# Kernel tuning notes

Measured on AMD Instinct MI355X. Metric: run time of the kernel, lower is better.

Reference implementation:

```python
import jax, jax.numpy as jnp
import numpy as np

B, L, DM, H, DK, DV = 8, 1024, 512, 8, 64, 64
LN_EPS = 1e-5

def setup_inputs() -> dict:
    key = jax.random.key(0)
    ks = jax.random.split(key, 8)
    s_in = 1.0 / np.sqrt(DM)
    return {
        "q": jax.random.normal(ks[0], (B, L, DM), jnp.float32),
        "k": jax.random.normal(ks[1], (B, L, DM), jnp.float32),
        "v": jax.random.normal(ks[2], (B, L, DM), jnp.float32),
        "Wq": jax.random.normal(ks[3], (DM, H * DK), jnp.float32) * s_in,
        "bq": jnp.zeros((H * DK,), jnp.float32),
        "Wk": jax.random.normal(ks[4], (DM, H * DK), jnp.float32) * s_in,
        "bk": jnp.zeros((H * DK,), jnp.float32),
        "Wv": jax.random.normal(ks[5], (DM, H * DV), jnp.float32) * s_in,
        "bv": jnp.zeros((H * DV,), jnp.float32),
        "Wmap": jax.random.normal(ks[6], (2 * DK, 1), jnp.float32) * (1.0 / np.sqrt(2 * DK)),
        "bmap": jnp.zeros((1,), jnp.float32),
        "Wfc": jax.random.normal(ks[7], (H * DV, DM), jnp.float32) * (1.0 / np.sqrt(H * DV)),
        "bfc": jnp.zeros((DM,), jnp.float32),
        "ln_scale": jnp.ones((DM,), jnp.float32),
        "ln_bias": jnp.zeros((DM,), jnp.float32),
    }

def reference(q, k, v, Wq, bq, Wk, bk, Wv, bv, Wmap, bmap, Wfc, bfc, ln_scale, ln_bias):
    sz_b, len_q, _ = q.shape
    len_k = k.shape[1]
    residual = q
    # projections -> (H, B, L, d)
    qh = (q @ Wq + bq).reshape(sz_b, len_q, H, DK).transpose(2, 0, 1, 3)
    kh = (k @ Wk + bk).reshape(sz_b, len_k, H, DK).transpose(2, 0, 1, 3)
    vh = (v @ Wv + bv).reshape(sz_b, len_k, H, DV).transpose(2, 0, 1, 3)
    # additive score: Linear(concat(q,k)) == q@Wmap[:DK] + k@Wmap[DK:] + b
    # (avoids materializing the (H*B, Lq, Lk, 2*DK) concat; same math)
    sq = qh @ Wmap[:DK, 0]   # (H, B, Lq)
    sk = kh @ Wmap[DK:, 0]   # (H, B, Lk)
    scores = sq[..., :, None] + sk[..., None, :] + bmap[0]  # (H, B, Lq, Lk)
    attn = jax.nn.softmax(scores, axis=-1)
    out = jnp.einsum('hbqk,hbkd->hbqd', attn, vh)            # (H, B, Lq, DV)
    out = out.transpose(1, 2, 0, 3).reshape(sz_b, len_q, H * DV)
    out = out @ Wfc + bfc + residual
    mu = out.mean(-1, keepdims=True)
    var = out.var(-1, keepdims=True)
    out = (out - mu) / jnp.sqrt(var + LN_EPS) * ln_scale + ln_bias
    return out, attn.reshape(H * sz_b, len_q, len_k)
```

## Files before the change

kernel.cpp:

```cpp
#include <hip/hip_runtime.h>
#include <cstdint>
#include <cstddef>

#define B 8
#define L 1024
#define DM 512
#define H 8
#define LN_EPS 1e-5f

#define U_OFF    0
#define SK_OFF   8192
#define PART_OFF 81920
#define CTX_OFF  344064
#define OBP_OFF  348160

#define OUT_ELEMS ((size_t)B * L * DM)

typedef float f4 __attribute__((ext_vector_type(4)));

__device__ __forceinline__ float wave_sum(float s) {
#pragma unroll
    for (int off = 32; off > 0; off >>= 1) s += __shfl_xor(s, off, 64);
    return s;
}

__global__ __launch_bounds__(64) void k_prep(const float* __restrict__ Wk,
                                             const float* __restrict__ Wmap,
                                             float* __restrict__ ws) {
    __shared__ float wm[64];
    int t = threadIdx.x;
    wm[t] = Wmap[64 + t];
    __syncthreads();
    int h = t >> 3, part = t & 7;
#pragma unroll
    for (int i = 0; i < 8; ++i) {
        int dm = blockIdx.x * 8 + i;
        const float* row = Wk + (size_t)dm * (H * 64) + h * 64 + part * 8;
        float s = 0.f;
#pragma unroll
        for (int d = 0; d < 8; ++d) s += row[d] * wm[part * 8 + d];
        s += __shfl_xor(s, 1, 64);
        s += __shfl_xor(s, 2, 64);
        s += __shfl_xor(s, 4, 64);
        if (part == 0) ws[U_OFF + dm * H + h] = s;
    }
}

__global__ __launch_bounds__(256) void k_sk(const float* __restrict__ k,
                                            float* __restrict__ ws) {
    int wave = threadIdx.x >> 6, lane = threadIdx.x & 63;
    int row = blockIdx.x * 4 + wave;
    int b = row >> 10, l = row & 1023;
    const float* krow = k + (size_t)row * DM;
    const float* u = ws + U_OFF;
    float acc[8] = {0, 0, 0, 0, 0, 0, 0, 0};
#pragma unroll
    for (int s8 = 0; s8 < 8; ++s8) {
        int dm = s8 * 64 + lane;
        float kv = krow[dm];
        const float4 ua = *(const float4*)(u + dm * 8);
        const float4 ub = *(const float4*)(u + dm * 8 + 4);
        acc[0] += kv * ua.x; acc[1] += kv * ua.y;
        acc[2] += kv * ua.z; acc[3] += kv * ua.w;
        acc[4] += kv * ub.x; acc[5] += kv * ub.y;
        acc[6] += kv * ub.z; acc[7] += kv * ub.w;
    }
#pragma unroll
    for (int off = 32; off > 0; off >>= 1) {
#pragma unroll
        for (int h = 0; h < 8; ++h) acc[h] += __shfl_xor(acc[h], off, 64);
    }
    float vout = 0.f;
#pragma unroll
    for (int h = 0; h < 8; ++h) if (lane == h) vout = acc[h];
    if (lane < 8)
        ws[SK_OFF + ((size_t)(lane * B + b)) * L + l] = vout;
}

__global__ __launch_bounds__(256) void k_vbar(const float* __restrict__ v,
                                              float* __restrict__ ws) {
    __shared__ float ps[H][128];
    int blk = blockIdx.x;
    int chunk = blk & 7, b = (blk >> 3) & 7, js = blk >> 6;
    int w = threadIdx.x >> 6, lane = threadIdx.x & 63;
#pragma unroll
    for (int rep = 0; rep < 2; ++rep) {
        int h = w * 2 + rep;
        const float* rowp = ws + SK_OFF + ((size_t)(h * B + b)) * L;
        float e[16];
        const f4* r4 = (const f4*)(rowp + lane * 16);
        float part = 0.f;
#pragma unroll
        for (int i = 0; i < 4; ++i) {
            f4 x = r4[i];
            e[i * 4 + 0] = __expf(x.x); e[i * 4 + 1] = __expf(x.y);
            e[i * 4 + 2] = __expf(x.z); e[i * 4 + 3] = __expf(x.w);
            part += e[i * 4 + 0] + e[i * 4 + 1] + e[i * 4 + 2] + e[i * 4 + 3];
        }
        float s = wave_sum(part);
        float inv = 1.f / s;
        float2 seg = *(const float2*)(rowp + js * 128 + lane * 2);
        ps[h][lane * 2 + 0] = __expf(seg.x) * inv;
        ps[h][lane * 2 + 1] = __expf(seg.y) * inv;
    }
    __syncthreads();
    int dm = chunk * 64 + lane;
    const float* vb0 = v + ((size_t)b * L + js * 128) * DM + dm;
    int h0 = w * 2;
    float a0 = 0.f, a1 = 0.f;
#pragma unroll 4
    for (int jj = 0; jj < 128; ++jj) {
        float vv = vb0[(size_t)jj * DM];
        a0 += ps[h0][jj] * vv;
        a1 += ps[h0 + 1][jj] * vv;
    }
    ws[PART_OFF + ((size_t)((js * H + h0) * B + b)) * DM + dm] = a0;
    ws[PART_OFF + ((size_t)((js * H + h0 + 1) * B + b)) * DM + dm] = a1;
}

__global__ __launch_bounds__(256) void k_ctx(const float* __restrict__ Wv,
                                             const float* __restrict__ bv,
                                             float* __restrict__ ws) {
    __shared__ float vb[DM];
    __shared__ float red[4][64];
    int hb = blockIdx.x;
    int h = hb >> 3, b = hb & 7;
#pragma unroll
    for (int it = 0; it < 2; ++it) {
        int dm = threadIdx.x + it * 256;
        float s = 0.f;
#pragma unroll
        for (int js = 0; js < 8; ++js)
            s += ws[PART_OFF + ((size_t)((js * H + h) * B + b)) * DM + dm];
        vb[dm] = s;
    }
    __syncthreads();
    int w = threadIdx.x >> 6, d = threadIdx.x & 63;
    float acc = 0.f;
#pragma unroll 4
    for (int i = 0; i < 128; ++i) {
        int dm = w * 128 + i;
        acc += vb[dm] * Wv[(size_t)dm * DM + h * 64 + d];
    }
    red[w][d] = acc;
    __syncthreads();
    if (w == 0) {
        float r = red[0][d] + red[1][d] + red[2][d] + red[3][d] + bv[h * 64 + d];
        ws[CTX_OFF + (size_t)b * DM + h * 64 + d] = r;
    }
}

__global__ __launch_bounds__(512) void k_obase(const float* __restrict__ Wfc,
                                               float* __restrict__ ws) {
    __shared__ float cxs[64];
    int b = blockIdx.x & 7, ms = blockIdx.x >> 3;
    if (threadIdx.x < 64)
        cxs[threadIdx.x] = ws[CTX_OFF + (size_t)b * DM + ms * 64 + threadIdx.x];
    __syncthreads();
    int n = threadIdx.x;
    float acc = 0.f;
#pragma unroll 4
    for (int m = 0; m < 64; ++m)
        acc += cxs[m] * Wfc[(size_t)(ms * 64 + m) * DM + n];
    ws[OBP_OFF + (size_t)(ms * B + b) * DM + n] = acc;
}

__global__ __launch_bounds__(256) void k_out(const float* __restrict__ q,
                                             const float* __restrict__ bfc,
                                             const float* __restrict__ lns,
                                             const float* __restrict__ lnb,
                                             const float* __restrict__ ws,
                                             float* __restrict__ out) {
    __shared__ float obf[DM];
    int b = blockIdx.x >> 8;
    for (int i = threadIdx.x; i < DM; i += 256) {
        float s = bfc[i];
#pragma unroll
        for (int ms = 0; ms < 8; ++ms)
            s += ws[OBP_OFF + (size_t)(ms * B + b) * DM + i];
        obf[i] = s;
    }
    __syncthreads();
    int wave = threadIdx.x >> 6, lane = threadIdx.x & 63;
    int row = blockIdx.x * 4 + wave;
    const float* qr = q + (size_t)row * DM;
    int d0 = lane * 8;
    float4 a = *(const float4*)(qr + d0);
    float4 c = *(const float4*)(qr + d0 + 4);
    float x[8] = {a.x + obf[d0],     a.y + obf[d0 + 1],
                  a.z + obf[d0 + 2], a.w + obf[d0 + 3],
                  c.x + obf[d0 + 4], c.y + obf[d0 + 5],
                  c.z + obf[d0 + 6], c.w + obf[d0 + 7]};
    float sum = 0.f, sq = 0.f;
#pragma unroll
    for (int i = 0; i < 8; ++i) { sum += x[i]; sq += x[i] * x[i]; }
#pragma unroll
    for (int off = 32; off > 0; off >>= 1) {
        sum += __shfl_xor(sum, off, 64);
        sq  += __shfl_xor(sq,  off, 64);
    }
    float mu = sum * (1.f / DM);
    float var = sq * (1.f / DM) - mu * mu;
    float inv = rsqrtf(var + LN_EPS);
    float4 sa = *(const float4*)(lns + d0);
    float4 sc = *(const float4*)(lns + d0 + 4);
    float4 ba = *(const float4*)(lnb + d0);
    float4 bb = *(const float4*)(lnb + d0 + 4);
    float sarr[8] = {sa.x, sa.y, sa.z, sa.w, sc.x, sc.y, sc.z, sc.w};
    float barr[8] = {ba.x, ba.y, ba.z, ba.w, bb.x, bb.y, bb.z, bb.w};
    float y[8];
#pragma unroll
    for (int i = 0; i < 8; ++i) y[i] = (x[i] - mu) * inv * sarr[i] + barr[i];
    float4 o0 = {y[0], y[1], y[2], y[3]};
    float4 o1 = {y[4], y[5], y[6], y[7]};
    *(float4*)(out + (size_t)row * DM + d0) = o0;
    *(float4*)(out + (size_t)row * DM + d0 + 4) = o1;
}

__global__ __launch_bounds__(256) void k_attn(const float* __restrict__ ws,
                                              float* __restrict__ out) {
    __shared__ float red[4];
    int hb = blockIdx.x >> 6;
    int ic = blockIdx.x & 63;
    int t = threadIdx.x, wave = t >> 6, lane = t & 63;
    float4 s4 = *(const float4*)&ws[SK_OFF + (size_t)hb * L + t * 4];
    float e0 = __expf(s4.x), e1 = __expf(s4.y), e2 = __expf(s4.z), e3 = __expf(s4.w);
    float s = wave_sum(e0 + e1 + e2 + e3);
    if (lane == 0) red[wave] = s;
    __syncthreads();
    float inv = 1.f / (red[0] + red[1] + red[2] + red[3]);
    f4 p4 = {e0 * inv, e1 * inv, e2 * inv, e3 * inv};
    float* base = out + OUT_ELEMS + ((size_t)hb * L + (size_t)ic * 16) * L + t * 4;
#pragma unroll
    for (int r = 0; r < 16; ++r)
        __builtin_nontemporal_store(p4, (f4*)(base + (size_t)r * L));
}

extern "C" void kernel_launch(void* const* d_in, const int* in_sizes, int n_in,
                              void* d_out, int out_size, void* d_ws, size_t ws_size,
                              hipStream_t stream) {
    const float* q    = (const float*)d_in[0];
    const float* k    = (const float*)d_in[1];
    const float* v    = (const float*)d_in[2];
    const float* Wk   = (const float*)d_in[5];
    const float* Wv   = (const float*)d_in[7];
    const float* bv   = (const float*)d_in[8];
    const float* Wmap = (const float*)d_in[9];
    const float* Wfc  = (const float*)d_in[11];
    const float* bfc  = (const float*)d_in[12];
    const float* lns  = (const float*)d_in[13];
    const float* lnb  = (const float*)d_in[14];
    float* out = (float*)d_out;
    float* ws  = (float*)d_ws;

    hipLaunchKernelGGL(k_prep,  dim3(64),   dim3(64),  0, stream, Wk, Wmap, ws);
    hipLaunchKernelGGL(k_sk,    dim3(2048), dim3(256), 0, stream, k, ws);
    hipLaunchKernelGGL(k_vbar,  dim3(512),  dim3(256), 0, stream, v, ws);
    hipLaunchKernelGGL(k_ctx,   dim3(64),   dim3(256), 0, stream, Wv, bv, ws);
    hipLaunchKernelGGL(k_obase, dim3(64),   dim3(512), 0, stream, Wfc, ws);
    hipLaunchKernelGGL(k_out,   dim3(2048), dim3(256), 0, stream, q, bfc, lns, lnb, ws, out);
    hipLaunchKernelGGL(k_attn,  dim3(4096), dim3(256), 0, stream, ws, out);
}
```

Before: 110.6 us.

## Fuse vbar, ctx, obase, out and attn into one persistent kernel with atomic counters

Merges five dependent kernels into a single launch. Block ranges run different stages, and dependent stages spin on global atomic counters set by earlier block groups. The streaming attention-matrix write blocks sit between the producer and the final LayerNorm blocks, so their memory traffic can overlap the small serial GEMV chain. This removes launch gaps. In exchange it relies on blocks being dispatched in index order to avoid deadlock, and it adds spin-wait latency. The LayerNorm blocks now handle 16 rows each instead of 4.

```diff
diff --git a/kernel.cpp b/kernel.cpp
--- a/kernel.cpp
+++ b/kernel.cpp
@@ -9,6 +9,7 @@
 #define LN_EPS 1e-5f
 
 #define U_OFF    0
+#define CNT_OFF  4096
 #define SK_OFF   8192
 #define PART_OFF 81920
 #define CTX_OFF  344064
@@ -22,6 +23,20 @@
 #pragma unroll
     for (int off = 32; off > 0; off >>= 1) s += __shfl_xor(s, off, 64);
     return s;
+}
+
+__device__ __forceinline__ void wait_cnt(int* cnt, int target) {
+    if (threadIdx.x == 0) {
+        while (__hip_atomic_load(cnt, __ATOMIC_RELAXED, __HIP_MEMORY_SCOPE_AGENT) < target)
+            __builtin_amdgcn_s_sleep(8);
+    }
+    __syncthreads();
+    __builtin_amdgcn_fence(__ATOMIC_ACQUIRE, "agent");
+}
+__device__ __forceinline__ void signal_cnt(int* cnt) {
+    __syncthreads();
+    if (threadIdx.x == 0)
+        __hip_atomic_fetch_add(cnt, 1, __ATOMIC_RELEASE, __HIP_MEMORY_SCOPE_AGENT);
 }
 
 __global__ __launch_bounds__(64) void k_prep(const float* __restrict__ Wk,
@@ -29,6 +44,7 @@
                                              float* __restrict__ ws) {
     __shared__ float wm[64];
     int t = threadIdx.x;
+    if (blockIdx.x == 0 && t < 3) ((int*)(ws + CNT_OFF))[t] = 0;
     wm[t] = Wmap[64 + t];
     __syncthreads();
     int h = t >> 3, part = t & 7;
@@ -77,163 +93,158 @@
         ws[SK_OFF + ((size_t)(lane * B + b)) * L + l] = vout;
 }
 
-__global__ __launch_bounds__(256) void k_vbar(const float* __restrict__ v,
-                                              float* __restrict__ ws) {
-    __shared__ float ps[H][128];
+__global__ __launch_bounds__(256) void k_mega(
+    const float* __restrict__ q, const float* __restrict__ v,
+    const float* __restrict__ Wv, const float* __restrict__ bv,
+    const float* __restrict__ Wfc, const float* __restrict__ bfc,
+    const float* __restrict__ lns, const float* __restrict__ lnb,
+    float* __restrict__ ws, float* __restrict__ out)
+{
+    __shared__ float smem[1032];
+    int* cnt = (int*)(ws + CNT_OFF);
     int blk = blockIdx.x;
-    int chunk = blk & 7, b = (blk >> 3) & 7, js = blk >> 6;
-    int w = threadIdx.x >> 6, lane = threadIdx.x & 63;
-#pragma unroll
-    for (int rep = 0; rep < 2; ++rep) {
-        int h = w * 2 + rep;
-        const float* rowp = ws + SK_OFF + ((size_t)(h * B + b)) * L;
-        float e[16];
-        const f4* r4 = (const f4*)(rowp + lane * 16);
-        float part = 0.f;
-#pragma unroll
-        for (int i = 0; i < 4; ++i) {
-            f4 x = r4[i];
-            e[i * 4 + 0] = __expf(x.x); e[i * 4 + 1] = __expf(x.y);
-            e[i * 4 + 2] = __expf(x.z); e[i * 4 + 3] = __expf(x.w);
-            part += e[i * 4 + 0] + e[i * 4 + 1] + e[i * 4 + 2] + e[i * 4 + 3];
-        }
-        float s = wave_sum(part);
-        float inv = 1.f / s;
-        float2 seg = *(const float2*)(rowp + js * 128 + lane * 2);
-        ps[h][lane * 2 + 0] = __expf(seg.x) * inv;
-        ps[h][lane * 2 + 1] = __expf(seg.y) * inv;
-    }
-    __syncthreads();
-    int dm = chunk * 64 + lane;
-    const float* vb0 = v + ((size_t)b * L + js * 128) * DM + dm;
-    int h0 = w * 2;
-    float a0 = 0.f, a1 = 0.f;
+    int t = threadIdx.x, wave = t >> 6, lane = t & 63;
+
+    if (blk < 512) {
+        int chunk = blk & 7, b = (blk >> 3) & 7, js = blk >> 6;
+#pragma unroll
+        for (int rep = 0; rep < 2; ++rep) {
+            int h = wave * 2 + rep;
+            const float* rowp = ws + SK_OFF + ((size_t)(h * B + b)) * L;
+            const f4* r4 = (const f4*)(rowp + lane * 16);
+            float part = 0.f;
+#pragma unroll
+            for (int i = 0; i < 4; ++i) {
+                f4 x = r4[i];
+                part += __expf(x.x) + __expf(x.y) + __expf(x.z) + __expf(x.w);
+            }
+            float s = wave_sum(part);
+            float inv = 1.f / s;
+            float2 seg = *(const float2*)(rowp + js * 128 + lane * 2);
+            smem[h * 128 + lane * 2 + 0] = __expf(seg.x) * inv;
+            smem[h * 128 + lane * 2 + 1] = __expf(seg.y) * inv;
+        }
+        __syncthreads();
+        int dm = chunk * 64 + lane;
+        const float* vb0 = v + ((size_t)b * L + js * 128) * DM + dm;
+        int h0 = wave * 2;
+        float a0 = 0.f, a1 = 0.f;
 #pragma unroll 4
-    for (int jj = 0; jj < 128; ++jj) {
-        float vv = vb0[(size_t)jj * DM];
-        a0 += ps[h0][jj] * vv;
-        a1 += ps[h0 + 1][jj] * vv;
-    }
-    ws[PART_OFF + ((size_t)((js * H + h0) * B + b)) * DM + dm] = a0;
-    ws[PART_OFF + ((size_t)((js * H + h0 + 1) * B + b)) * DM + dm] = a1;
-}
-
-__global__ __launch_bounds__(256) void k_ctx(const float* __restrict__ Wv,
-                                             const float* __restrict__ bv,
-                                             float* __restrict__ ws) {
-    __shared__ float vb[DM];
-    __shared__ float red[4][64];
-    int hb = blockIdx.x;
-    int h = hb >> 3, b = hb & 7;
-#pragma unroll
-    for (int it = 0; it < 2; ++it) {
-        int dm = threadIdx.x + it * 256;
-        float s = 0.f;
-#pragma unroll
-        for (int js = 0; js < 8; ++js)
-            s += ws[PART_OFF + ((size_t)((js * H + h) * B + b)) * DM + dm];
-        vb[dm] = s;
-    }
-    __syncthreads();
-    int w = threadIdx.x >> 6, d = threadIdx.x & 63;
-    float acc = 0.f;
+        for (int jj = 0; jj < 128; ++jj) {
+            float vv = vb0[(size_t)jj * DM];
+            a0 += smem[h0 * 128 + jj] * vv;
+            a1 += smem[(h0 + 1) * 128 + jj] * vv;
+        }
+        ws[PART_OFF + ((size_t)((js * H + h0) * B + b)) * DM + dm] = a0;
+        ws[PART_OFF + ((size_t)((js * H + h0 + 1) * B + b)) * DM + dm] = a1;
+        signal_cnt(cnt + 0);
+    } else if (blk < 576) {
+        wait_cnt(cnt + 0, 512);
+        int hb = blk - 512;
+        int h = hb >> 3, b = hb & 7;
+#pragma unroll
+        for (int it = 0; it < 2; ++it) {
+            int dm = t + it * 256;
+            float s = 0.f;
+#pragma unroll
+            for (int js = 0; js < 8; ++js)
+                s += ws[PART_OFF + ((size_t)((js * H + h) * B + b)) * DM + dm];
+            smem[dm] = s;
+        }
+        __syncthreads();
+        float acc = 0.f;
 #pragma unroll 4
-    for (int i = 0; i < 128; ++i) {
-        int dm = w * 128 + i;
-        acc += vb[dm] * Wv[(size_t)dm * DM + h * 64 + d];
-    }
-    red[w][d] = acc;
-    __syncthreads();
-    if (w == 0) {
-        float r = red[0][d] + red[1][d] + red[2][d] + red[3][d] + bv[h * 64 + d];
-        ws[CTX_OFF + (size_t)b * DM + h * 64 + d] = r;
-    }
-}
-
-__global__ __launch_bounds__(512) void k_obase(const float* __restrict__ Wfc,
-                                               float* __restrict__ ws) {
-    __shared__ float cxs[64];
-    int b = blockIdx.x & 7, ms = blockIdx.x >> 3;
-    if (threadIdx.x < 64)
-        cxs[threadIdx.x] = ws[CTX_OFF + (size_t)b * DM + ms * 64 + threadIdx.x];
-    __syncthreads();
-    int n = threadIdx.x;
-    float acc = 0.f;
+        for (int i = 0; i < 128; ++i) {
+            int dm = wave * 128 + i;
+            acc += smem[dm] * Wv[(size_t)dm * DM + h * 64 + lane];
+        }
+        smem[512 + wave * 64 + lane] = acc;
+        __syncthreads();
+        if (wave == 0) {
+            float r = smem[512 + lane] + smem[576 + lane] + smem[640 + lane]
+                    + smem[704 + lane] + bv[h * 64 + lane];
+            ws[CTX_OFF + (size_t)b * DM + h * 64 + lane] = r;
+        }
+        signal_cnt(cnt + 1);
+    } else if (blk < 640) {
+        wait_cnt(cnt + 1, 64);
+        int idx = blk - 576;
+        int b = idx & 7, ms = idx >> 3;
+        if (t < 64) smem[t] = ws[CTX_OFF + (size_t)b * DM + ms * 64 + t];
+        __syncthreads();
+#pragma unroll
+        for (int it = 0; it < 2; ++it) {
+            int n = t + it * 256;
+            float acc = 0.f;
 #pragma unroll 4
-    for (int m = 0; m < 64; ++m)
-        acc += cxs[m] * Wfc[(size_t)(ms * 64 + m) * DM + n];
-    ws[OBP_OFF + (size_t)(ms * B + b) * DM + n] = acc;
-}
-
-__global__ __launch_bounds__(256) void k_out(const float* __restrict__ q,
-                                             const float* __restrict__ bfc,
-                                             const float* __restrict__ lns,
-                                             const float* __restrict__ lnb,
-                                             const float* __restrict__ ws,
-                                             float* __restrict__ out) {
-    __shared__ float obf[DM];
-    int b = blockIdx.x >> 8;
-    for (int i = threadIdx.x; i < DM; i += 256) {
-        float s = bfc[i];
-#pragma unroll
-        for (int ms = 0; ms < 8; ++ms)
-            s += ws[OBP_OFF + (size_t)(ms * B + b) * DM + i];
-        obf[i] = s;
-    }
-    __syncthreads();
-    int wave = threadIdx.x >> 6, lane = threadIdx.x & 63;
-    int row = blockIdx.x * 4 + wave;
-    const float* qr = q + (size_t)row * DM;
-    int d0 = lane * 8;
-    float4 a = *(const float4*)(qr + d0);
-    float4 c = *(const float4*)(qr + d0 + 4);
-    float x[8] = {a.x + obf[d0],     a.y + obf[d0 + 1],
-                  a.z + obf[d0 + 2], a.w + obf[d0 + 3],
-                  c.x + obf[d0 + 4], c.y + obf[d0 + 5],
-                  c.z + obf[d0 + 6], c.w + obf[d0 + 7]};
-    float sum = 0.f, sq = 0.f;
-#pragma unroll
-    for (int i = 0; i < 8; ++i) { sum += x[i]; sq += x[i] * x[i]; }
-#pragma unroll
-    for (int off = 32; off > 0; off >>= 1) {
-        sum += __shfl_xor(sum, off, 64);
-        sq  += __shfl_xor(sq,  off, 64);
-    }
-    float mu = sum * (1.f / DM);
-    float var = sq * (1.f / DM) - mu * mu;
-    float inv = rsqrtf(var + LN_EPS);
-    float4 sa = *(const float4*)(lns + d0);
-    float4 sc = *(const float4*)(lns + d0 + 4);
-    float4 ba = *(const float4*)(lnb + d0);
-    float4 bb = *(const float4*)(lnb + d0 + 4);
-    float sarr[8] = {sa.x, sa.y, sa.z, sa.w, sc.x, sc.y, sc.z, sc.w};
-    float barr[8] = {ba.x, ba.y, ba.z, ba.w, bb.x, bb.y, bb.z, bb.w};
-    float y[8];
-#pragma unroll
-    for (int i = 0; i < 8; ++i) y[i] = (x[i] - mu) * inv * sarr[i] + barr[i];
-    float4 o0 = {y[0], y[1], y[2], y[3]};
-    float4 o1 = {y[4], y[5], y[6], y[7]};
-    *(float4*)(out + (size_t)row * DM + d0) = o0;
-    *(float4*)(out + (size_t)row * DM + d0 + 4) = o1;
-}
-
-__global__ __launch_bounds__(256) void k_attn(const float* __restrict__ ws,
-                                              float* __restrict__ out) {
-    __shared__ float red[4];
-    int hb = blockIdx.x >> 6;
-    int ic = blockIdx.x & 63;
-    int t = threadIdx.x, wave = t >> 6, lane = t & 63;
-    float4 s4 = *(const float4*)&ws[SK_OFF + (size_t)hb * L + t * 4];
-    float e0 = __expf(s4.x), e1 = __expf(s4.y), e2 = __expf(s4.z), e3 = __expf(s4.w);
-    float s = wave_sum(e0 + e1 + e2 + e3);
-    if (lane == 0) red[wave] = s;
-    __syncthreads();
-    float inv = 1.f / (red[0] + red[1] + red[2] + red[3]);
-    f4 p4 = {e0 * inv, e1 * inv, e2 * inv, e3 * inv};
-    float* base = out + OUT_ELEMS + ((size_t)hb * L + (size_t)ic * 16) * L + t * 4;
-#pragma unroll
-    for (int r = 0; r < 16; ++r)
-        __builtin_nontemporal_store(p4, (f4*)(base + (size_t)r * L));
+            for (int m = 0; m < 64; ++m)
+                acc += smem[m] * Wfc[(size_t)(ms * 64 + m) * DM + n];
+            ws[OBP_OFF + (size_t)(ms * B + b) * DM + n] = acc;
+        }
+        signal_cnt(cnt + 2);
+    } else if (blk < 4736) {
+        int task = blk - 640;
+        int hb = task >> 6, ic = task & 63;
+        float4 s4 = *(const float4*)&ws[SK_OFF + (size_t)hb * L + t * 4];
+        float e0 = __expf(s4.x), e1 = __expf(s4.y), e2 = __expf(s4.z), e3 = __expf(s4.w);
+        float s = wave_sum(e0 + e1 + e2 + e3);
+        if (lane == 0) smem[1024 + wave] = s;
+        __syncthreads();
+        float inv = 1.f / (smem[1024] + smem[1025] + smem[1026] + smem[1027]);
+        f4 p4 = {e0 * inv, e1 * inv, e2 * inv, e3 * inv};
+        float* base = out + OUT_ELEMS + ((size_t)hb * L + (size_t)ic * 16) * L + t * 4;
+#pragma unroll
+        for (int r = 0; r < 16; ++r)
+            __builtin_nontemporal_store(p4, (f4*)(base + (size_t)r * L));
+    } else {
+        wait_cnt(cnt + 2, 64);
+        int rblk = blk - 4736;
+        int b = rblk >> 6;
+        for (int i = t; i < DM; i += 256) {
+            float s = bfc[i];
+#pragma unroll
+            for (int ms = 0; ms < 8; ++ms)
+                s += ws[OBP_OFF + (size_t)(ms * B + b) * DM + i];
+            smem[i] = s;
+        }
+        __syncthreads();
+#pragma unroll
+        for (int rep = 0; rep < 4; ++rep) {
+            int row = rblk * 16 + rep * 4 + wave;
+            const float* qr = q + (size_t)row * DM;
+            int d0 = lane * 8;
+            float4 a = *(const float4*)(qr + d0);
+            float4 c = *(const float4*)(qr + d0 + 4);
+            float x[8] = {a.x + smem[d0],     a.y + smem[d0 + 1],
+                          a.z + smem[d0 + 2], a.w + smem[d0 + 3],
+                          c.x + smem[d0 + 4], c.y + smem[d0 + 5],
+                          c.z + smem[d0 + 6], c.w + smem[d0 + 7]};
+            float sum = 0.f, sq = 0.f;
+#pragma unroll
+            for (int i = 0; i < 8; ++i) { sum += x[i]; sq += x[i] * x[i]; }
+#pragma unroll
+            for (int off = 32; off > 0; off >>= 1) {
+                sum += __shfl_xor(sum, off, 64);
+                sq  += __shfl_xor(sq,  off, 64);
+            }
+            float mu = sum * (1.f / DM);
+            float var = sq * (1.f / DM) - mu * mu;
+            float invs = rsqrtf(var + LN_EPS);
+            float4 sa = *(const float4*)(lns + d0);
+            float4 sc = *(const float4*)(lns + d0 + 4);
+            float4 ba = *(const float4*)(lnb + d0);
+            float4 bb = *(const float4*)(lnb + d0 + 4);
+            float sarr[8] = {sa.x, sa.y, sa.z, sa.w, sc.x, sc.y, sc.z, sc.w};
+            float barr[8] = {ba.x, ba.y, ba.z, ba.w, bb.x, bb.y, bb.z, bb.w};
+            float y[8];
+#pragma unroll
+            for (int i = 0; i < 8; ++i) y[i] = (x[i] - mu) * invs * sarr[i] + barr[i];
+            float4 o0 = {y[0], y[1], y[2], y[3]};
+            float4 o1 = {y[4], y[5], y[6], y[7]};
+            *(float4*)(out + (size_t)row * DM + d0) = o0;
+            *(float4*)(out + (size_t)row * DM + d0 + 4) = o1;
+        }
+    }
 }
 
 extern "C" void kernel_launch(void* const* d_in, const int* in_sizes, int n_in,
@@ -253,11 +264,8 @@
     float* out = (float*)d_out;
     float* ws  = (float*)d_ws;
 
-    hipLaunchKernelGGL(k_prep,  dim3(64),   dim3(64),  0, stream, Wk, Wmap, ws);
-    hipLaunchKernelGGL(k_sk,    dim3(2048), dim3(256), 0, stream, k, ws);
-    hipLaunchKernelGGL(k_vbar,  dim3(512),  dim3(256), 0, stream, v, ws);
-    hipLaunchKernelGGL(k_ctx,   dim3(64),   dim3(256), 0, stream, Wv, bv, ws);
-    hipLaunchKernelGGL(k_obase, dim3(64),   dim3(512), 0, stream, Wfc, ws);
-    hipLaunchKernelGGL(k_out,   dim3(2048), dim3(256), 0, stream, q, bfc, lns, lnb, ws, out);
-    hipLaunchKernelGGL(k_attn,  dim3(4096), dim3(256), 0, stream, ws, out);
-}
+    hipLaunchKernelGGL(k_prep, dim3(64),   dim3(64),  0, stream, Wk, Wmap, ws);
+    hipLaunchKernelGGL(k_sk,   dim3(2048), dim3(256), 0, stream, k, ws);
+    hipLaunchKernelGGL(k_mega, dim3(5248), dim3(256), 0, stream,
+                       q, v, Wv, bv, Wfc, bfc, lns, lnb, ws, out);
+}
```

Measured after the change: 168.2 us. 1.52x slower.

## Merge attention-map writes into dependent stages and fuse ctx/obase kernels

Applied to the files above, without the earlier changes.

The standalone attention-probability store kernel is split into chunks of tasks appended to the vbar, ctx/fc and layernorm kernels as extra blocks. The small, low-occupancy stages then run alongside the bandwidth-bound attention writes instead of serializing. The ctx and obase kernels are fused into one kernel, with each block redundantly computing the full context vector for its batch. The layernorm kernel now processes 16 rows per block. Seven launches drop to five. The risk is the redundant Wv GEMV work in each of the 64 blocks and load imbalance between the two block types in each kernel.

```diff
diff --git a/kernel.cpp b/kernel.cpp
--- a/kernel.cpp
+++ b/kernel.cpp
@@ -11,8 +11,7 @@
 #define U_OFF    0
 #define SK_OFF   8192
 #define PART_OFF 81920
-#define CTX_OFF  344064
-#define OBP_OFF  348160
+#define OB_OFF   344064
 
 #define OUT_ELEMS ((size_t)B * L * DM)
 
@@ -22,6 +21,23 @@
 #pragma unroll
     for (int off = 32; off > 0; off >>= 1) s += __shfl_xor(s, off, 64);
     return s;
+}
+
+__device__ __forceinline__ void attn_task(int task, const float* __restrict__ ws,
+                                          float* __restrict__ out, float* red) {
+    int hb = task >> 6, ic = task & 63;
+    int t = threadIdx.x, wave = t >> 6, lane = t & 63;
+    float4 s4 = *(const float4*)&ws[SK_OFF + (size_t)hb * L + t * 4];
+    float e0 = __expf(s4.x), e1 = __expf(s4.y), e2 = __expf(s4.z), e3 = __expf(s4.w);
+    float s = wave_sum(e0 + e1 + e2 + e3);
+    if (lane == 0) red[wave] = s;
+    __syncthreads();
+    float inv = 1.f / (red[0] + red[1] + red[2] + red[3]);
+    f4 p4 = {e0 * inv, e1 * inv, e2 * inv, e3 * inv};
+    float* base = out + OUT_ELEMS + ((size_t)hb * L + (size_t)ic * 16) * L + t * 4;
+#pragma unroll
+    for (int r = 0; r < 16; ++r)
+        __builtin_nontemporal_store(p4, (f4*)(base + (size_t)r * L));
 }
 
 __global__ __launch_bounds__(64) void k_prep(const float* __restrict__ Wk,
@@ -77,163 +93,153 @@
         ws[SK_OFF + ((size_t)(lane * B + b)) * L + l] = vout;
 }
 
-__global__ __launch_bounds__(256) void k_vbar(const float* __restrict__ v,
-                                              float* __restrict__ ws) {
-    __shared__ float ps[H][128];
+__global__ __launch_bounds__(256) void k_l3(const float* __restrict__ v,
+                                            float* __restrict__ ws,
+                                            float* __restrict__ out) {
+    __shared__ float smem[1028];
     int blk = blockIdx.x;
-    int chunk = blk & 7, b = (blk >> 3) & 7, js = blk >> 6;
-    int w = threadIdx.x >> 6, lane = threadIdx.x & 63;
-#pragma unroll
-    for (int rep = 0; rep < 2; ++rep) {
-        int h = w * 2 + rep;
-        const float* rowp = ws + SK_OFF + ((size_t)(h * B + b)) * L;
-        float e[16];
-        const f4* r4 = (const f4*)(rowp + lane * 16);
-        float part = 0.f;
-#pragma unroll
-        for (int i = 0; i < 4; ++i) {
-            f4 x = r4[i];
-            e[i * 4 + 0] = __expf(x.x); e[i * 4 + 1] = __expf(x.y);
-            e[i * 4 + 2] = __expf(x.z); e[i * 4 + 3] = __expf(x.w);
-            part += e[i * 4 + 0] + e[i * 4 + 1] + e[i * 4 + 2] + e[i * 4 + 3];
-        }
-        float s = wave_sum(part);
-        float inv = 1.f / s;
-        float2 seg = *(const float2*)(rowp + js * 128 + lane * 2);
-        ps[h][lane * 2 + 0] = __expf(seg.x) * inv;
-        ps[h][lane * 2 + 1] = __expf(seg.y) * inv;
-    }
-    __syncthreads();
-    int dm = chunk * 64 + lane;
-    const float* vb0 = v + ((size_t)b * L + js * 128) * DM + dm;
-    int h0 = w * 2;
-    float a0 = 0.f, a1 = 0.f;
+    int t = threadIdx.x, wave = t >> 6, lane = t & 63;
+    if (blk < 512) {
+        int chunk = blk & 7, b = (blk >> 3) & 7, js = blk >> 6;
+#pragma unroll
+        for (int rep = 0; rep < 2; ++rep) {
+            int h = wave * 2 + rep;
+            const float* rowp = ws + SK_OFF + ((size_t)(h * B + b)) * L;
+            const f4* r4 = (const f4*)(rowp + lane * 16);
+            float part = 0.f;
+#pragma unroll
+            for (int i = 0; i < 4; ++i) {
+                f4 x = r4[i];
+                part += __expf(x.x) + __expf(x.y) + __expf(x.z) + __expf(x.w);
+            }
+            float s = wave_sum(part);
+            float inv = 1.f / s;
+            float2 seg = *(const float2*)(rowp + js * 128 + lane * 2);
+            smem[h * 128 + lane * 2 + 0] = __expf(seg.x) * inv;
+            smem[h * 128 + lane * 2 + 1] = __expf(seg.y) * inv;
+        }
+        __syncthreads();
+        int dm = chunk * 64 + lane;
+        const float* vb0 = v + ((size_t)b * L + js * 128) * DM + dm;
+        int h0 = wave * 2;
+        float a0 = 0.f, a1 = 0.f;
 #pragma unroll 4
-    for (int jj = 0; jj < 128; ++jj) {
-        float vv = vb0[(size_t)jj * DM];
-        a0 += ps[h0][jj] * vv;
-        a1 += ps[h0 + 1][jj] * vv;
-    }
-    ws[PART_OFF + ((size_t)((js * H + h0) * B + b)) * DM + dm] = a0;
-    ws[PART_OFF + ((size_t)((js * H + h0 + 1) * B + b)) * DM + dm] = a1;
-}
-
-__global__ __launch_bounds__(256) void k_ctx(const float* __restrict__ Wv,
-                                             const float* __restrict__ bv,
-                                             float* __restrict__ ws) {
-    __shared__ float vb[DM];
+        for (int jj = 0; jj < 128; ++jj) {
+            float vv = vb0[(size_t)jj * DM];
+            a0 += smem[h0 * 128 + jj] * vv;
+            a1 += smem[(h0 + 1) * 128 + jj] * vv;
+        }
+        ws[PART_OFF + ((size_t)((js * H + h0) * B + b)) * DM + dm] = a0;
+        ws[PART_OFF + ((size_t)((js * H + h0 + 1) * B + b)) * DM + dm] = a1;
+    } else {
+        attn_task(blk - 512, ws, out, smem + 1024);
+    }
+}
+
+__global__ __launch_bounds__(256) void k_l4(const float* __restrict__ Wv,
+                                            const float* __restrict__ bv,
+                                            const float* __restrict__ Wfc,
+                                            const float* __restrict__ bfc,
+                                            float* __restrict__ ws,
+                                            float* __restrict__ out) {
+    __shared__ float vbs[4096];
+    __shared__ float ctxs[512];
     __shared__ float red[4][64];
-    int hb = blockIdx.x;
-    int h = hb >> 3, b = hb & 7;
-#pragma unroll
-    for (int it = 0; it < 2; ++it) {
-        int dm = threadIdx.x + it * 256;
-        float s = 0.f;
-#pragma unroll
-        for (int js = 0; js < 8; ++js)
-            s += ws[PART_OFF + ((size_t)((js * H + h) * B + b)) * DM + dm];
-        vb[dm] = s;
-    }
-    __syncthreads();
-    int w = threadIdx.x >> 6, d = threadIdx.x & 63;
-    float acc = 0.f;
+    int blk = blockIdx.x;
+    int t = threadIdx.x;
+    if (blk < 64) {
+        int b = blk >> 3, ns = blk & 7;
+        for (int i = t; i < 4096; i += 256) {
+            int h = i >> 9, dm = i & 511;
+            float s = 0.f;
+#pragma unroll
+            for (int js = 0; js < 8; ++js)
+                s += ws[PART_OFF + ((size_t)((js * H + h) * B + b)) * DM + dm];
+            vbs[i] = s;
+        }
+        __syncthreads();
+#pragma unroll
+        for (int mo = 0; mo < 2; ++mo) {
+            int m = t + mo * 256;
+            const float* vh = &vbs[(m >> 6) << 9];
+            float acc = bv[m];
 #pragma unroll 4
-    for (int i = 0; i < 128; ++i) {
-        int dm = w * 128 + i;
-        acc += vb[dm] * Wv[(size_t)dm * DM + h * 64 + d];
-    }
-    red[w][d] = acc;
-    __syncthreads();
-    if (w == 0) {
-        float r = red[0][d] + red[1][d] + red[2][d] + red[3][d] + bv[h * 64 + d];
-        ws[CTX_OFF + (size_t)b * DM + h * 64 + d] = r;
-    }
-}
-
-__global__ __launch_bounds__(512) void k_obase(const float* __restrict__ Wfc,
-                                               float* __restrict__ ws) {
-    __shared__ float cxs[64];
-    int b = blockIdx.x & 7, ms = blockIdx.x >> 3;
-    if (threadIdx.x < 64)
-        cxs[threadIdx.x] = ws[CTX_OFF + (size_t)b * DM + ms * 64 + threadIdx.x];
-    __syncthreads();
-    int n = threadIdx.x;
-    float acc = 0.f;
+            for (int dm = 0; dm < DM; ++dm)
+                acc += vh[dm] * Wv[(size_t)dm * DM + m];
+            ctxs[m] = acc;
+        }
+        __syncthreads();
+        int seg = t >> 6, nl = t & 63;
+        int n = ns * 64 + nl;
+        float acc = 0.f;
 #pragma unroll 4
-    for (int m = 0; m < 64; ++m)
-        acc += cxs[m] * Wfc[(size_t)(ms * 64 + m) * DM + n];
-    ws[OBP_OFF + (size_t)(ms * B + b) * DM + n] = acc;
-}
-
-__global__ __launch_bounds__(256) void k_out(const float* __restrict__ q,
-                                             const float* __restrict__ bfc,
-                                             const float* __restrict__ lns,
-                                             const float* __restrict__ lnb,
-                                             const float* __restrict__ ws,
-                                             float* __restrict__ out) {
-    __shared__ float obf[DM];
-    int b = blockIdx.x >> 8;
-    for (int i = threadIdx.x; i < DM; i += 256) {
-        float s = bfc[i];
-#pragma unroll
-        for (int ms = 0; ms < 8; ++ms)
-            s += ws[OBP_OFF + (size_t)(ms * B + b) * DM + i];
-        obf[i] = s;
-    }
-    __syncthreads();
-    int wave = threadIdx.x >> 6, lane = threadIdx.x & 63;
-    int row = blockIdx.x * 4 + wave;
-    const float* qr = q + (size_t)row * DM;
-    int d0 = lane * 8;
-    float4 a = *(const float4*)(qr + d0);
-    float4 c = *(const float4*)(qr + d0 + 4);
-    float x[8] = {a.x + obf[d0],     a.y + obf[d0 + 1],
-                  a.z + obf[d0 + 2], a.w + obf[d0 + 3],
-                  c.x + obf[d0 + 4], c.y + obf[d0 + 5],
-                  c.z + obf[d0 + 6], c.w + obf[d0 + 7]};
-    float sum = 0.f, sq = 0.f;
-#pragma unroll
-    for (int i = 0; i < 8; ++i) { sum += x[i]; sq += x[i] * x[i]; }
-#pragma unroll
-    for (int off = 32; off > 0; off >>= 1) {
-        sum += __shfl_xor(sum, off, 64);
-        sq  += __shfl_xor(sq,  off, 64);
-    }
-    float mu = sum * (1.f / DM);
-    float var = sq * (1.f / DM) - mu * mu;
-    float inv = rsqrtf(var + LN_EPS);
-    float4 sa = *(const float4*)(lns + d0);
-    float4 sc = *(const float4*)(lns + d0 + 4);
-    float4 ba = *(const float4*)(lnb + d0);
-    float4 bb = *(const float4*)(lnb + d0 + 4);
-    float sarr[8] = {sa.x, sa.y, sa.z, sa.w, sc.x, sc.y, sc.z, sc.w};
-    float barr[8] = {ba.x, ba.y, ba.z, ba.w, bb.x, bb.y, bb.z, bb.w};
-    float y[8];
-#pragma unroll
-    for (int i = 0; i < 8; ++i) y[i] = (x[i] - mu) * inv * sarr[i] + barr[i];
-    float4 o0 = {y[0], y[1], y[2], y[3]};
-    float4 o1 = {y[4], y[5], y[6], y[7]};
-    *(float4*)(out + (size_t)row * DM + d0) = o0;
-    *(float4*)(out + (size_t)row * DM + d0 + 4) = o1;
-}
-
-__global__ __launch_bounds__(256) void k_attn(const float* __restrict__ ws,
-                                              float* __restrict__ out) {
-    __shared__ float red[4];
-    int hb = blockIdx.x >> 6;
-    int ic = blockIdx.x & 63;
+        for (int i = 0; i < 128; ++i) {
+            int m = seg * 128 + i;
+            acc += ctxs[m] * Wfc[(size_t)m * DM + n];
+        }
+        red[seg][nl] = acc;
+        __syncthreads();
+        if (seg == 0) {
+            float r = red[0][nl] + red[1][nl] + red[2][nl] + red[3][nl] + bfc[n];
+            ws[OB_OFF + (size_t)b * DM + n] = r;
+        }
+    } else {
+        attn_task(1408 + (blk - 64), ws, out, &red[0][0]);
+    }
+}
+
+__global__ __launch_bounds__(256) void k_l5(const float* __restrict__ q,
+                                            const float* __restrict__ lns,
+                                            const float* __restrict__ lnb,
+                                            float* __restrict__ ws,
+                                            float* __restrict__ out) {
+    __shared__ float obf[516];
+    int blk = blockIdx.x;
     int t = threadIdx.x, wave = t >> 6, lane = t & 63;
-    float4 s4 = *(const float4*)&ws[SK_OFF + (size_t)hb * L + t * 4];
-    float e0 = __expf(s4.x), e1 = __expf(s4.y), e2 = __expf(s4.z), e3 = __expf(s4.w);
-    float s = wave_sum(e0 + e1 + e2 + e3);
-    if (lane == 0) red[wave] = s;
-    __syncthreads();
-    float inv = 1.f / (red[0] + red[1] + red[2] + red[3]);
-    f4 p4 = {e0 * inv, e1 * inv, e2 * inv, e3 * inv};
-    float* base = out + OUT_ELEMS + ((size_t)hb * L + (size_t)ic * 16) * L + t * 4;
-#pragma unroll
-    for (int r = 0; r < 16; ++r)
-        __builtin_nontemporal_store(p4, (f4*)(base + (size_t)r * L));
+    if (blk < 512) {
+        int b = blk >> 6;
+        for (int i = t; i < DM; i += 256)
+            obf[i] = ws[OB_OFF + (size_t)b * DM + i];
+        __syncthreads();
+#pragma unroll
+        for (int rep = 0; rep < 4; ++rep) {
+            int row = blk * 16 + rep * 4 + wave;
+            const float* qr = q + (size_t)row * DM;
+            int d0 = lane * 8;
+            float4 a = *(const float4*)(qr + d0);
+            float4 c = *(const float4*)(qr + d0 + 4);
+            float x[8] = {a.x + obf[d0],     a.y + obf[d0 + 1],
+                          a.z + obf[d0 + 2], a.w + obf[d0 + 3],
+                          c.x + obf[d0 + 4], c.y + obf[d0 + 5],
+                          c.z + obf[d0 + 6], c.w + obf[d0 + 7]};
+            float sum = 0.f, sq = 0.f;
+#pragma unroll
+            for (int i = 0; i < 8; ++i) { sum += x[i]; sq += x[i] * x[i]; }
+#pragma unroll
+            for (int off = 32; off > 0; off >>= 1) {
+                sum += __shfl_xor(sum, off, 64);
+                sq  += __shfl_xor(sq,  off, 64);
+            }
+            float mu = sum * (1.f / DM);
+            float var = sq * (1.f / DM) - mu * mu;
+            float invs = rsqrtf(var + LN_EPS);
+            float4 sa = *(const float4*)(lns + d0);
+            float4 sc = *(const float4*)(lns + d0 + 4);
+            float4 ba = *(const float4*)(lnb + d0);
+            float4 bb = *(const float4*)(lnb + d0 + 4);
+            float sarr[8] = {sa.x, sa.y, sa.z, sa.w, sc.x, sc.y, sc.z, sc.w};
+            float barr[8] = {ba.x, ba.y, ba.z, ba.w, bb.x, bb.y, bb.z, bb.w};
+            float y[8];
+#pragma unroll
+            for (int i = 0; i < 8; ++i) y[i] = (x[i] - mu) * invs * sarr[i] + barr[i];
+            float4 o0 = {y[0], y[1], y[2], y[3]};
+            float4 o1 = {y[4], y[5], y[6], y[7]};
+            *(float4*)(out + (size_t)row * DM + d0) = o0;
+            *(float4*)(out + (size_t)row * DM + d0 + 4) = o1;
+        }
+    } else {
+        attn_task(2816 + (blk - 512), ws, out, obf + 512);
+    }
 }
 
 extern "C" void kernel_launch(void* const* d_in, const int* in_sizes, int n_in,
@@ -253,11 +259,9 @@
     float* out = (float*)d_out;
     float* ws  = (float*)d_ws;
 
-    hipLaunchKernelGGL(k_prep,  dim3(64),   dim3(64),  0, stream, Wk, Wmap, ws);
-    hipLaunchKernelGGL(k_sk,    dim3(2048), dim3(256), 0, stream, k, ws);
-    hipLaunchKernelGGL(k_vbar,  dim3(512),  dim3(256), 0, stream, v, ws);
-    hipLaunchKernelGGL(k_ctx,   dim3(64),   dim3(256), 0, stream, Wv, bv, ws);
-    hipLaunchKernelGGL(k_obase, dim3(64),   dim3(512), 0, stream, Wfc, ws);
-    hipLaunchKernelGGL(k_out,   dim3(2048), dim3(256), 0, stream, q, bfc, lns, lnb, ws, out);
-    hipLaunchKernelGGL(k_attn,  dim3(4096), dim3(256), 0, stream, ws, out);
-}
+    hipLaunchKernelGGL(k_prep, dim3(64),   dim3(64),  0, stream, Wk, Wmap, ws);
+    hipLaunchKernelGGL(k_sk,   dim3(2048), dim3(256), 0, stream, k, ws);
+    hipLaunchKernelGGL(k_l3,   dim3(1920), dim3(256), 0, stream, v, ws, out);
+    hipLaunchKernelGGL(k_l4,   dim3(1472), dim3(256), 0, stream, Wv, bv, Wfc, bfc, ws, out);
+    hipLaunchKernelGGL(k_l5,   dim3(1792), dim3(256), 0, stream, q, lns, lnb, ws, out);
+}
```

Result: slower. 149.4 us (+35.0%).
